# Kernel optimization log

Measured on AMD Instinct MI355X. Metric: run time of the kernel, lower is better.

The kernel has to match this reference:

```python
import jax, jax.numpy as jnp
import numpy as np

NPOINT, RADIUS, NSAMPLE = 1024, 0.2, 32


def _fps(xyz, npoint):
    # xyz: (B, N, 3) -> (B, npoint) int32, iterative furthest point sampling
    B, N, _ = xyz.shape

    def step(carry, _):
        dists, far = carry  # (B,N), (B,)
        centroid = jnp.take_along_axis(xyz, far[:, None, None], axis=1)  # (B,1,3)
        d = jnp.sum((xyz - centroid) ** 2, axis=-1)  # (B,N)
        dists = jnp.minimum(dists, d)
        nxt = jnp.argmax(dists, axis=-1).astype(jnp.int32)
        return (dists, nxt), far

    init = (jnp.full((B, N), 1e10, xyz.dtype), jnp.zeros((B,), jnp.int32))
    _, idx = jax.lax.scan(step, init, None, length=npoint)
    return jnp.transpose(idx)  # (B, npoint)


def _ball_query(radius, nsample, xyz, new_xyz):
    # xyz: (B,N,3), new_xyz: (B,S,3) -> (B,S,nsample) int32
    N = xyz.shape[1]
    d2 = jnp.sum((new_xyz[:, :, None, :] - xyz[:, None, :, :]) ** 2, axis=-1)  # (B,S,N)
    # first-nsample-in-range semantics of PointNet++ ball_query
    key = jnp.where(d2 < radius * radius, jnp.arange(N, dtype=jnp.int32), N)
    neg, order = jax.lax.top_k(-key, nsample)  # smallest keys first
    valid = (-neg) < N
    return jnp.where(valid, order, order[..., :1])  # pad with first valid idx


def _group(feat, idx):
    # feat: (B,D,N), idx: (B,S,ns) -> (B,D,S,ns)
    return jax.vmap(lambda f, i: f[:, i])(feat, idx)


def _conv(x, w, b):
    # 1x1 Conv2d: x (B,C,S,ns), w (O,C), b (O)
    return jnp.einsum('oc,bcps->bops', w, x) + b[None, :, None, None]


def _bn(x, s, t):
    # inference BatchNorm folded into per-channel affine
    return x * s[None, :, None, None] + t[None, :, None, None]


def setup_inputs() -> dict:
    key = jax.random.key(0)
    ks = jax.random.split(key, 40)
    B, N, D = 16, 8192, 64
    BCH = 8  # max(8, 64 // 8)

    def w(k, shape, scale=0.1):
        return jax.random.normal(k, shape, jnp.float32) * scale

    def bn(k, c):
        k1, k2 = jax.random.split(k)
        return (jax.random.uniform(k1, (c,), jnp.float32, 0.75, 1.25),
                0.1 * jax.random.normal(k2, (c,), jnp.float32))

    attn_s0, attn_t0 = bn(ks[2], BCH)
    attn_s1, attn_t1 = bn(ks[3], D)
    attn_s2, attn_t2 = bn(ks[4], D)
    mlp_s0, mlp_t0 = bn(ks[5], 64)
    mlp_s1, mlp_t1 = bn(ks[6], 64)
    eca_s, eca_t = bn(ks[7], 128)
    return {
        'xyz': jax.random.uniform(ks[0], (B, 3, N), jnp.float32),
        'points': jax.random.normal(ks[1], (B, D, N), jnp.float32),
        'attn_w0': w(ks[10], (BCH, 3)), 'attn_b0': w(ks[11], (BCH,)),
        'attn_s0': attn_s0, 'attn_t0': attn_t0,
        'attn_w1': w(ks[12], (D, BCH)), 'attn_b1': w(ks[13], (D,)),
        'attn_s1': attn_s1, 'attn_t1': attn_t1,
        'attn_w2': w(ks[14], (D, D)), 'attn_b2': w(ks[15], (D,)),
        'attn_s2': attn_s2, 'attn_t2': attn_t2,
        'mlp_w0': w(ks[16], (64, D)), 'mlp_b0': w(ks[17], (64,)),
        'mlp_s0': mlp_s0, 'mlp_t0': mlp_t0,
        'mlp_w1': w(ks[18], (64, 64)), 'mlp_b1': w(ks[19], (64,)),
        'mlp_s1': mlp_s1, 'mlp_t1': mlp_t1,
        'eca_k': w(ks[20], (3,), 0.5),
        'eca_w': w(ks[21], (128, 64)), 'eca_b': w(ks[22], (128,)),
        'eca_s': eca_s, 'eca_t': eca_t,
    }


def reference(xyz, points,
              attn_w0, attn_b0, attn_s0, attn_t0,
              attn_w1, attn_b1, attn_s1, attn_t1,
              attn_w2, attn_b2, attn_s2, attn_t2,
              mlp_w0, mlp_b0, mlp_s0, mlp_t0,
              mlp_w1, mlp_b1, mlp_s1, mlp_t1,
              eca_k, eca_w, eca_b, eca_s, eca_t):
    xyz_f = jnp.transpose(xyz, (0, 2, 1))  # (B,N,3)
    # 1. sampling + grouping
    fps_idx = _fps(xyz_f, NPOINT)  # (B,S)
    new_xyz = jax.vmap(lambda p, i: p[:, i])(xyz, fps_idx)  # (B,3,S)
    idx = _ball_query(RADIUS, NSAMPLE, xyz_f, jnp.transpose(new_xyz, (0, 2, 1)))
    grouped_xyz = _group(xyz, idx) - new_xyz[..., None]  # (B,3,S,ns)
    x = _group(points, idx)  # (B,D,S,ns)
    # 2. position-attention module
    pos = jax.nn.relu(_bn(_conv(grouped_xyz, attn_w0, attn_b0), attn_s0, attn_t0))
    pos = _bn(_conv(pos, attn_w1, attn_b1), attn_s1, attn_t1)
    x = x + pos
    x = _bn(_conv(x, attn_w2, attn_b2), attn_s2, attn_t2)
    # 3. shared MLP (conv-bn-relu over mlp[:-1])
    x = jax.nn.relu(_bn(_conv(x, mlp_w0, mlp_b0), mlp_s0, mlp_t0))
    x = jax.nn.relu(_bn(_conv(x, mlp_w1, mlp_b1), mlp_s1, mlp_t1))
    # 4. ECA channel attention + final 1x1 conv-bn
    y = jnp.mean(x, axis=(2, 3))  # (B,C)
    yp = jnp.pad(y, ((0, 0), (1, 1)))
    y = eca_k[0] * yp[:, :-2] + eca_k[1] * yp[:, 1:-1] + eca_k[2] * yp[:, 2:]
    x = x * jax.nn.sigmoid(y)[:, :, None, None]
    x = _bn(_conv(x, eca_w, eca_b), eca_s, eca_t)
    # 5. max-pool over neighborhood
    new_features = jnp.max(x, axis=-1)  # (B,128,S)
    return (new_xyz, new_features)
```

## Files before the change

### kernel.cpp

```cpp
#include <hip/hip_runtime.h>

typedef unsigned int   u32;
typedef unsigned long long u64;
typedef float pkf2 __attribute__((ext_vector_type(2)));

#define B_  16
#define N_  8192
#define S_  1024
#define NS_ 32
#define XS_ 68
#define NWORK_ 240
#define NCHUNK_ 4096

__device__ __forceinline__ float nanguard(float v) {
  u32 x = __float_as_uint(v);
  if ((x & 0x7F80u) == 0x7F80u) x ^= 0x0080u;
  return __uint_as_float(x);
}

__device__ __forceinline__ float wave_max_nonneg(float v) {
  int x = __float_as_int(v);
#define DPP_STEP(ctrl) \
  x = __float_as_int(fmaxf(__int_as_float(x), \
      __int_as_float(__builtin_amdgcn_update_dpp(0, x, (ctrl), 0xf, 0xf, true))))
  DPP_STEP(0x111);
  DPP_STEP(0x112);
  DPP_STEP(0x114);
  DPP_STEP(0x118);
  DPP_STEP(0x142);
  DPP_STEP(0x143);
#undef DPP_STEP
  return __int_as_float(__builtin_amdgcn_readlane(x, 63));
}

__global__ __launch_bounds__(256) void k_xyzt(const float* __restrict__ xyz, float4* __restrict__ xyzt,
                                              u32* __restrict__ prog) {
  if (blockIdx.x == 0 && blockIdx.y == 0 && threadIdx.x < 16) prog[threadIdx.x] = 0u;
  int b = blockIdx.y;
  int i = blockIdx.x * 256 + threadIdx.x;
  const float* p = xyz + (size_t)b * 3 * N_;
  xyzt[(size_t)b * N_ + i] = make_float4(p[i], p[N_ + i], p[2 * N_ + i], 0.f);
}

__global__ __launch_bounds__(256) void k_ptst(const float* __restrict__ pts, float* __restrict__ ptst) {
  __shared__ float tile[64][65];
  int b = blockIdx.y, n0 = blockIdx.x * 64, t = threadIdx.x;
  {
    int c = t >> 2, j0 = (t & 3) * 16;
    const float4* src = (const float4*)(pts + (size_t)b * 64 * N_ + (size_t)c * N_ + n0 + j0);
#pragma unroll
    for (int q = 0; q < 4; ++q) {
      float4 a = src[q];
      tile[c][j0 + 4*q + 0] = a.x; tile[c][j0 + 4*q + 1] = a.y;
      tile[c][j0 + 4*q + 2] = a.z; tile[c][j0 + 4*q + 3] = a.w;
    }
  }
  __syncthreads();
  {
    int n = t >> 2, c0 = (t & 3) * 16;
    float4* dv = (float4*)(ptst + ((size_t)b * N_ + n0 + n) * 64 + c0);
#pragma unroll
    for (int q = 0; q < 4; ++q)
      dv[q] = make_float4(tile[c0 + 4*q + 0][n], tile[c0 + 4*q + 1][n],
                          tile[c0 + 4*q + 2][n], tile[c0 + 4*q + 3][n]);
  }
}

__global__ __launch_bounds__(1024)
__attribute__((amdgpu_waves_per_eu(4, 4)))
void k_fps(const float4* __restrict__ xyzt,
           float4* __restrict__ nxf,
           float* __restrict__ out_xyz) {
#pragma clang fp contract(off)
  __shared__ float4 ldsp[N_];
  __shared__ u64 slot[4];
  __shared__ int win_hist[S_];
  int b = blockIdx.x, t = threadIdx.x;
  const float4* p4 = xyzt + (size_t)b * N_;
  const float4* pp8 = p4 + t * 8;

  float4 q0 = pp8[0], q1 = pp8[1], q2 = pp8[2], q3 = pp8[3];
  float4 q4 = pp8[4], q5 = pp8[5], q6 = pp8[6], q7 = pp8[7];
  ldsp[t * 8 + 0] = q0; ldsp[t * 8 + 1] = q1; ldsp[t * 8 + 2] = q2; ldsp[t * 8 + 3] = q3;
  ldsp[t * 8 + 4] = q4; ldsp[t * 8 + 5] = q5; ldsp[t * 8 + 6] = q6; ldsp[t * 8 + 7] = q7;

#define DECLPAIR(P, A, B) \
  pkf2 px##P = {q##A.x, q##B.x}; pkf2 py##P = {q##A.y, q##B.y}; \
  pkf2 pz##P = {q##A.z, q##B.z}; pkf2 dm##P = {1e10f, 1e10f};
  DECLPAIR(01, 0, 1) DECLPAIR(23, 2, 3) DECLPAIR(45, 4, 5) DECLPAIR(67, 6, 7)
#undef DECLPAIR
#define PIN(P) asm volatile("" : "+v"(px##P), "+v"(py##P), "+v"(pz##P));
  PIN(01) PIN(23) PIN(45) PIN(67)
#undef PIN

  if (t == 0) {
    slot[0] = 8191ull;
    slot[1] = 0; slot[2] = 0; slot[3] = 0;
    win_hist[0] = 0;
  }
  __syncthreads();
  int lane = t & 63;
  for (int it = 1; it < S_; ++it) {
    u64 w = slot[(it - 1) & 3];
    int widx = 8191 - (int)(w & 0xFFFFFFFFull);
    if (t == 0) { win_hist[it - 1] = widx; slot[(it + 1) & 3] = 0; }
    float4 c = ldsp[widx & (N_ - 1)];
    pkf2 cx2 = {c.x, c.x}, cy2 = {c.y, c.y}, cz2 = {c.z, c.z};
#define UPDP(P) { \
    pkf2 dx = px##P - cx2; pkf2 dy = py##P - cy2; pkf2 dz = pz##P - cz2; \
    pkf2 xx = dx * dx; pkf2 yy = dy * dy; pkf2 zz = dz * dz; \
    pkf2 ss = xx + yy; pkf2 dd = ss + zz; \
    dm##P.x = fminf(dm##P.x, dd.x); dm##P.y = fminf(dm##P.y, dd.y); }
    UPDP(01) UPDP(23) UPDP(45) UPDP(67)
#undef UPDP
    float e0 = dm01.x, e1 = dm01.y, e2 = dm23.x, e3 = dm23.y;
    float e4 = dm45.x, e5 = dm45.y, e6 = dm67.x, e7 = dm67.y;
    float va0 = e1 > e0 ? e1 : e0; int ia0 = e1 > e0 ? 1 : 0;
    float va1 = e3 > e2 ? e3 : e2; int ia1 = e3 > e2 ? 3 : 2;
    float va2 = e5 > e4 ? e5 : e4; int ia2 = e5 > e4 ? 5 : 4;
    float va3 = e7 > e6 ? e7 : e6; int ia3 = e7 > e6 ? 7 : 6;
// ... 151 lines not shown

  {
    int n = t >> 3, cc = t & 7;
    const float* gx = &sm.scratch[256 + n * 4];
    float a = sm.bb0[cc];
    a += sm.W0f[cc * 4 + 0] * gx[0];
    a += sm.W0f[cc * 4 + 1] * gx[1];
    a += sm.W0f[cc * 4 + 2] * gx[2];
    sm.scratch[n * 8 + cc] = fmaxf(a, 0.f);
  }
  {
#pragma unroll
    for (int nj = 0; nj < 8; ++nj) {
      float a = sm.bb1[lane];
      const float* p8 = &sm.scratch[(n0 + nj) * 8];
#pragma unroll
      for (int k = 0; k < 8; ++k) a += sm.W1f[lane * 9 + k] * p8[k];
      sm.X[(n0 + nj) * XS_ + lane] += a;
    }
  }
  gemm64<false>(sm.Wbuf, sm.X, sm.H, sm.s2f, sm.bb2, lane, n0);
  __syncthreads();
  stage_w64(sm.Wbuf, m0w, t);
  __syncthreads();
  gemm64<true>(sm.Wbuf, sm.H, sm.X, sm.sm0f, sm.bm0, lane, n0);
  __syncthreads();
  stage_w64(sm.Wbuf, m1w, t);
  __syncthreads();
  gemm64<true>(sm.Wbuf, sm.X, sm.H, sm.sm1f, sm.bm1, lane, n0);
}

template<bool USE_PTST, bool WRITE_H2>
__global__ __launch_bounds__(256) void k_chain(
    const float4* __restrict__ xyzt, const float* __restrict__ ptst,
    const float* __restrict__ points,
    const float4* __restrict__ nxf, const int* __restrict__ ballidx,
    const float* w0, const float* b0, const float* s0, const float* t0,
    const float* w1, const float* b1, const float* s1, const float* t1,
    const float* w2, const float* b2, const float* s2, const float* t2,
    const float* m0w, const float* m0b, const float* m0s, const float* m0t,
    const float* m1w, const float* m1b, const float* m1s, const float* m1t,
    float* __restrict__ h2out, float* __restrict__ partials) {
  __shared__ ChainSm sm;
  int t = threadIdx.x, bs = blockIdx.x;
  int b = bs >> 10, s = bs & 1023;
  int lane = t & 63, g = t >> 6, n0 = g * 8;

  chain_tile<USE_PTST>(sm, b, s, bs, xyzt, ptst, points, nxf, ballidx,
                       w0, b0, s0, t0, w1, b1, s1, t1, w2, b2, s2, t2,
                       m0w, m0b, m0s, m0t, m1w, m1b, m1s, m1t);

  float* psum = sm.scratch;
  float lsum = 0.f;
#pragma unroll
  for (int nj = 0; nj < 8; ++nj) {
    float r = sm.H[(n0 + nj) * XS_ + lane];
    lsum += r;
    if (WRITE_H2)
      h2out[((size_t)bs * 32 + n0 + nj) * 64 + lane] = r;
  }
  psum[lane * 5 + g] = lsum;
  __syncthreads();
  if (t < 64) {
    float v = (psum[t * 5 + 0] + psum[t * 5 + 1]) + (psum[t * 5 + 2] + psum[t * 5 + 3]);
    partials[(size_t)bs * 64 + t] = v;
  }
}

struct ChainSub {
  float X[32 * XS_];
  float H[32 * XS_];
  float scratch[384];
  int   idx_s[NS_];
};
struct WkSm {
  float Wc2[64 * XS_];
  float Wm0[64 * XS_];
  float Wm1[64 * XS_];
  float W1f[64 * 9];
  float W0f[8 * 4];
  float s2f[64], sm0f[64], sm1f[64];
  float bb0[8];
  float bb1[64], bb2[64], bm0[64], bm1[64];
  ChainSub sub[4];
};
struct FpsSm {
  float4 ldsp[N_];
  u64 slot[4];
  int win_hist[S_];
};
union FusedSm { FpsSm f; WkSm w; };
static_assert(sizeof(FusedSm) <= 160 * 1024, "LDS overflow");

__global__ __launch_bounds__(1024)
__attribute__((amdgpu_waves_per_eu(4, 4)))
void k_fused(const float4* __restrict__ xyzt, const float* __restrict__ ptst,
             float4* __restrict__ nxf, float* __restrict__ out_xyz,
             u32* __restrict__ prog,
             const float* w0, const float* b0, const float* s0, const float* t0,
             const float* w1, const float* b1, const float* s1, const float* t1,
             const float* w2, const float* b2, const float* s2, const float* t2,
             const float* m0w, const float* m0b, const float* m0s, const float* m0t,
             const float* m1w, const float* m1b, const float* m1s, const float* m1t,
             float* __restrict__ h2out, float* __restrict__ partials) {
  __shared__ FusedSm smu;
  int t = threadIdx.x;

  if (blockIdx.x < B_) {
#pragma clang fp contract(off)
    FpsSm& fs = smu.f;
    int b = blockIdx.x;
    const float4* p4 = xyzt + (size_t)b * N_;
    const float4* pp8 = p4 + t * 8;

    float4 q0 = pp8[0], q1 = pp8[1], q2 = pp8[2], q3 = pp8[3];
    float4 q4 = pp8[4], q5 = pp8[5], q6 = pp8[6], q7 = pp8[7];
    fs.ldsp[t * 8 + 0] = q0; fs.ldsp[t * 8 + 1] = q1; fs.ldsp[t * 8 + 2] = q2; fs.ldsp[t * 8 + 3] = q3;
    fs.ldsp[t * 8 + 4] = q4; fs.ldsp[t * 8 + 5] = q5; fs.ldsp[t * 8 + 6] = q6; fs.ldsp[t * 8 + 7] = q7;

#define DECLPAIR(P, A, B) \
    pkf2 px##P = {q##A.x, q##B.x}; pkf2 py##P = {q##A.y, q##B.y}; \
    pkf2 pz##P = {q##A.z, q##B.z}; pkf2 dm##P = {1e10f, 1e10f};
    DECLPAIR(01, 0, 1) DECLPAIR(23, 2, 3) DECLPAIR(45, 4, 5) DECLPAIR(67, 6, 7)
#undef DECLPAIR
#define PIN(P) asm volatile("" : "+v"(px##P), "+v"(py##P), "+v"(pz##P));
    PIN(01) PIN(23) PIN(45) PIN(67)
#undef PIN

    if (t == 0) {
      fs.slot[0] = 8191ull;
      fs.slot[1] = 0; fs.slot[2] = 0; fs.slot[3] = 0;
      fs.win_hist[0] = 0;
    }
    __syncthreads();
    int lane = t & 63;
    for (int it = 1; it < S_; ++it) {
      u64 w = fs.slot[(it - 1) & 3];
      int widx = 8191 - (int)(w & 0xFFFFFFFFull);
      float4 c = fs.ldsp[widx & (N_ - 1)];
      if (t == 0) {
        fs.win_hist[it - 1] = widx; fs.slot[(it + 1) & 3] = 0;
        if ((it & 15) == 0)
          __hip_atomic_store(&prog[b], (u32)(it - 1), __ATOMIC_RELEASE, __HIP_MEMORY_SCOPE_AGENT);
        nxf[(size_t)b * S_ + (it - 1)] = c;
      }
      pkf2 cx2 = {c.x, c.x}, cy2 = {c.y, c.y}, cz2 = {c.z, c.z};
#define UPDP(P) { \
      pkf2 dx = px##P - cx2; pkf2 dy = py##P - cy2; pkf2 dz = pz##P - cz2; \
      pkf2 xx = dx * dx; pkf2 yy = dy * dy; pkf2 zz = dz * dz; \
      pkf2 ss = xx + yy; pkf2 dd = ss + zz; \
      dm##P.x = fminf(dm##P.x, dd.x); dm##P.y = fminf(dm##P.y, dd.y); }
      UPDP(01) UPDP(23) UPDP(45) UPDP(67)
#undef UPDP
      float e0 = dm01.x, e1 = dm01.y, e2 = dm23.x, e3 = dm23.y;
      float e4 = dm45.x, e5 = dm45.y, e6 = dm67.x, e7 = dm67.y;
      float va0 = e1 > e0 ? e1 : e0; int ia0 = e1 > e0 ? 1 : 0;
      float va1 = e3 > e2 ? e3 : e2; int ia1 = e3 > e2 ? 3 : 2;
      float va2 = e5 > e4 ? e5 : e4; int ia2 = e5 > e4 ? 5 : 4;
      float va3 = e7 > e6 ? e7 : e6; int ia3 = e7 > e6 ? 7 : 6;
      float vb0 = va1 > va0 ? va1 : va0; int ib0 = va1 > va0 ? ia1 : ia0;
      float vb1 = va3 > va2 ? va3 : va2; int ib1 = va3 > va2 ? ia3 : ia2;
      float bv = vb1 > vb0 ? vb1 : vb0;  int bk = vb1 > vb0 ? ib1 : ib0;
      int bi = t * 8 + bk;
      float wm = wave_max_nonneg(bv);
      u64 msk = __ballot(bv == wm);
      int wl = __ffsll((long long)msk) - 1;
      int wbi = __builtin_amdgcn_readlane(bi, wl);
      if (lane == 0)
        atomicMax(&fs.slot[it & 3],
                  ((u64)__float_as_uint(wm) << 32) | (u64)(u32)(8191 - wbi));
      __syncthreads();
    }
    if (t == 0) {
      int wl_ = 8191 - (int)(fs.slot[(S_ - 1) & 3] & 0xFFFFFFFFull);
      fs.win_hist[S_ - 1] = wl_;
      float4 c = fs.ldsp[wl_ & (N_ - 1)];
      nxf[(size_t)b * S_ + (S_ - 1)] = c;
    }
    __syncthreads();
    {
      int wi = fs.win_hist[t] & (N_ - 1);
      float4 c = fs.ldsp[wi];
      float* o = out_xyz + (size_t)b * 3 * S_;
      o[t] = nanguard(c.x); o[S_ + t] = nanguard(c.y); o[2 * S_ + t] = nanguard(c.z);
    }
    if (t == 0)
      __hip_atomic_store(&prog[b], (u32)S_, __ATOMIC_RELEASE, __HIP_MEMORY_SCOPE_AGENT);
    return;
  }

  WkSm& wk = smu.w;
  int w = blockIdx.x - B_;
  if (t < 256) {
    stage_w64(wk.Wc2, w2, t);
    stage_w64(wk.Wm0, m0w, t);
    stage_w64(wk.Wm1, m1w, t);
  }
  if (t < 64) {
    float v2 = s2[t];  wk.s2f[t] = v2;  wk.bb2[t] = v2 * b2[t] + t2[t];
    float vm0 = m0s[t]; wk.sm0f[t] = vm0; wk.bm0[t] = vm0 * m0b[t] + m0t[t];
    float vm1 = m1s[t]; wk.sm1f[t] = vm1; wk.bm1[t] = vm1 * m1b[t] + m1t[t];
    float v1 = s1[t];
#pragma unroll
    for (int k = 0; k < 8; ++k) wk.W1f[t * 9 + k] = v1 * w1[t * 8 + k];
    wk.bb1[t] = v1 * b1[t] + t1[t];
  }
  if (t < 8) {
    float v0 = s0[t];
#pragma unroll
    for (int k = 0; k < 3; ++k) wk.W0f[t * 4 + k] = v0 * w0[t * 3 + k];
    wk.bb0[t] = v0 * b0[t] + t0[t];
  }
  __syncthreads();

  int sg = t >> 8, tid = t & 255, lane = t & 63, g2 = (t >> 6) & 3, n0 = g2 * 8;
  ChainSub& cs = wk.sub[sg];

  for (int c = w; c < NCHUNK_; c += NWORK_) {
    int s = c >> 2, bg = c & 3, b = bg * 4 + sg;
    if (t == 0) {
      int bbase = bg * 4;
#pragma unroll
      for (int j = 0; j < 4; ++j) {
        while (__hip_atomic_load(&prog[bbase + j], __ATOMIC_RELAXED, __HIP_MEMORY_SCOPE_AGENT) < (u32)(s + 1))
          __builtin_amdgcn_s_sleep(32);
      }
      (void)__hip_atomic_load(&prog[bbase], __ATOMIC_ACQUIRE, __HIP_MEMORY_SCOPE_AGENT);
    }
    __syncthreads();

    float4 cc;
    if (g2 == 0) {
      cc = nxf[(size_t)b * S_ + s];
      const float4* pts = xyzt + (size_t)b * N_;
      int cnt = 0, first = 0;
      bool havefirst = false;
      for (int chunk = 0; chunk < N_; chunk += 64) {
        float4 p = pts[chunk + lane];
        float dx = p.x - cc.x, dy = p.y - cc.y, dz = p.z - cc.z;
        float d2 = __fadd_rn(__fadd_rn(__fmul_rn(dx, dx), __fmul_rn(dy, dy)), __fmul_rn(dz, dz));
        bool v = d2 <= 0.04f;
        u64 m = __ballot(v);
        if (m) {
          int pos = cnt + __popcll(m & ((1ull << lane) - 1ull));
          if (v && pos < NS_) cs.idx_s[pos] = chunk + lane;
          if (!havefirst) { first = chunk + (__ffsll((long long)m) - 1); havefirst = true; }
          cnt += __popcll(m);
          if (cnt >= NS_) break;
        }
      }
      if (cnt < NS_) {
        for (int p = cnt + lane; p < NS_; p += 64) cs.idx_s[p] = first;
      }
    }
    __syncthreads();

    {
      int n = tid >> 3, c8 = (tid & 7) * 8;
      int pi = cs.idx_s[n];
      const float4* v = (const float4*)(ptst + ((size_t)b * N_ + pi) * 64 + c8);
      float4* xr = (float4*)&cs.X[n * XS_ + c8];
      xr[0] = v[0]; xr[1] = v[1];
    }
    if (tid < NS_) {
      float4 p = xyzt[(size_t)b * N_ + cs.idx_s[tid]];
      float* gx = &cs.scratch[256 + tid * 4];
      gx[0] = p.x - cc.x; gx[1] = p.y - cc.y; gx[2] = p.z - cc.z;
    }
    __syncthreads();

    {
      int n = tid >> 3, ch = tid & 7;
      const float* gx = &cs.scratch[256 + n * 4];
      float a = wk.bb0[ch];
      a += wk.W0f[ch * 4 + 0] * gx[0];
      a += wk.W0f[ch * 4 + 1] * gx[1];
      a += wk.W0f[ch * 4 + 2] * gx[2];
      cs.scratch[n * 8 + ch] = fmaxf(a, 0.f);
    }
    {
#pragma unroll
      for (int nj = 0; nj < 8; ++nj) {
        float a = wk.bb1[lane];
        const float* p8 = &cs.scratch[(n0 + nj) * 8];
#pragma unroll
        for (int k = 0; k < 8; ++k) a += wk.W1f[lane * 9 + k] * p8[k];
        cs.X[(n0 + nj) * XS_ + lane] += a;
      }
    }
    gemm64<false>(wk.Wc2, cs.X, cs.H, wk.s2f, wk.bb2, lane, n0);
    gemm64<true >(wk.Wm0, cs.H, cs.X, wk.sm0f, wk.bm0, lane, n0);
    gemm64<true >(wk.Wm1, cs.X, cs.H, wk.sm1f, wk.bm1, lane, n0);

    int bs = (b << 10) | s;
    float lsum = 0.f;
#pragma unroll
    for (int nj = 0; nj < 8; ++nj) {
      float r = cs.H[(n0 + nj) * XS_ + lane];
      lsum += r;
      h2out[((size_t)bs * 32 + n0 + nj) * 64 + lane] = r;
    }
    __syncthreads();
    cs.scratch[lane * 5 + g2] = lsum;
    __syncthreads();
    if (tid < 64) {
      float v = (cs.scratch[tid * 5 + 0] + cs.scratch[tid * 5 + 1]) +
                (cs.scratch[tid * 5 + 2] + cs.scratch[tid * 5 + 3]);
      partials[(size_t)bs * 64 + tid] = v;
    }
  }
}

__global__ __launch_bounds__(256) void k_eca(const float* __restrict__ partials,
                                             const float* __restrict__ ecak,
                                             float* __restrict__ sig) {
  __shared__ float red[64 * 5];
  __shared__ float yy[66];
  int b = blockIdx.x, t = threadIdx.x;
  int c = t & 63, sg = t >> 6;
  float acc = 0.f;
  for (int s = sg; s < S_; s += 4) acc += partials[((size_t)b * S_ + s) * 64 + c];
  red[c * 5 + sg] = acc;
  __syncthreads();
  if (t < 64) {
    float v = (red[t * 5 + 0] + red[t * 5 + 1]) + (red[t * 5 + 2] + red[t * 5 + 3]);
    yy[t + 1] = v * (1.f / 32768.f);
  }
  if (t == 64) { yy[0] = 0.f; yy[65] = 0.f; }
  __syncthreads();
  if (t < 64) {
    float gv = ecak[0] * yy[t] + ecak[1] * yy[t + 1] + ecak[2] * yy[t + 2];
    sig[b * 64 + t] = 1.f / (1.f + expf(-gv));
  }
}

__device__ __forceinline__ void final_gemm(const float* __restrict__ WA,
                                           const float* __restrict__ WB,
                                           const float* __restrict__ X2,
                                           const float* __restrict__ esf,
                                           const float* __restrict__ bbf,
                                           float* __restrict__ zred,
                                           float* __restrict__ outf,
                                           int b, int s, int t) {
  int lane = t & 63, g = t >> 6, n0 = g * 8;
  float aA[8] = {0,0,0,0,0,0,0,0}, aB[8] = {0,0,0,0,0,0,0,0};
#pragma unroll
  for (int k4 = 0; k4 < 16; ++k4) {
    float4 wqA = *(const float4*)&WA[lane * XS_ + k4 * 4];
    float4 wqB = *(const float4*)&WB[lane * XS_ + k4 * 4];
#pragma unroll
    for (int nj = 0; nj < 8; ++nj) {
      float4 xq = *(const float4*)&X2[(n0 + nj) * XS_ + k4 * 4];
      aA[nj] += wqA.x * xq.x; aA[nj] += wqA.y * xq.y;
      aA[nj] += wqA.z * xq.z; aA[nj] += wqA.w * xq.w;
      aB[nj] += wqB.x * xq.x; aB[nj] += wqB.y * xq.y;
      aB[nj] += wqB.z * xq.z; aB[nj] += wqB.w * xq.w;
    }
  }
  float mA = aA[0], mB = aB[0];
#pragma unroll
  for (int j = 1; j < 8; ++j) { mA = fmaxf(mA, aA[j]); mB = fmaxf(mB, aB[j]); }
  zred[lane * 5 + g]        = esf[lane] * mA + bbf[lane];
  zred[(lane + 64) * 5 + g] = esf[lane + 64] * mB + bbf[lane + 64];
  __syncthreads();
  if (t < 128) {
    float m = fmaxf(fmaxf(zred[t * 5 + 0], zred[t * 5 + 1]),
                    fmaxf(zred[t * 5 + 2], zred[t * 5 + 3]));
    outf[((size_t)b * 128 + t) * S_ + s] = nanguard(m);
  }
}

__global__ __launch_bounds__(256) void k_final_h2(const float* __restrict__ h2,
                                                  const float* __restrict__ sig,
                                                  const float* ew, const float* eb,
                                                  const float* es, const float* et,
                                                  float* __restrict__ outf) {
  __shared__ float Wh[128 * XS_];
  __shared__ float esf[128], bbf[128], sigl[64];
  __shared__ float X2[32 * XS_];
  __shared__ float zred[128 * 5];
  int t = threadIdx.x, bs = blockIdx.x;
  int b = bs >> 10, s = bs & 1023;
  {
    int c2 = t >> 1, h = (t & 1) * 32;
    const float4* src = (const float4*)(ew + c2 * 64 + h);
    float4* dst = (float4*)(Wh + c2 * XS_ + h);
#pragma unroll
    for (int j = 0; j < 8; ++j) dst[j] = src[j];
  }
  if (t < 128) {
    float v = es[t]; esf[t] = v; bbf[t] = v * eb[t] + et[t];
  }
  if (t < 64) sigl[t] = sig[b * 64 + t];
  __syncthreads();
  {
    int n = t >> 3, c8 = (t & 7) * 8;
    const float4* v = (const float4*)(h2 + ((size_t)bs * 32 + n) * 64 + c8);
    float4 a = v[0], bq = v[1];
    a.x *= sigl[c8 + 0]; a.y *= sigl[c8 + 1]; a.z *= sigl[c8 + 2]; a.w *= sigl[c8 + 3];
    bq.x *= sigl[c8 + 4]; bq.y *= sigl[c8 + 5]; bq.z *= sigl[c8 + 6]; bq.w *= sigl[c8 + 7];
    float4* xr = (float4*)&X2[n * XS_ + c8];
    xr[0] = a; xr[1] = bq;
  }
  final_gemm(Wh, Wh + 64 * XS_, X2, esf, bbf, zred, outf, b, s, t);
}

template<bool USE_PTST>
__global__ __launch_bounds__(256) void k_final_rec(
    const float4* __restrict__ xyzt, const float* __restrict__ ptst,
    const float* __restrict__ points,
    const float4* __restrict__ nxf, const int* __restrict__ ballidx,
    const float* w0, const float* b0, const float* s0, const float* t0,
    const float* w1, const float* b1, const float* s1, const float* t1,
    const float* w2, const float* b2, const float* s2, const float* t2,
    const float* m0w, const float* m0b, const float* m0s, const float* m0t,
    const float* m1w, const float* m1b, const float* m1s, const float* m1t,
    const float* __restrict__ sig,
    const float* ew, const float* eb, const float* es, const float* et,
    float* __restrict__ outf) {
  __shared__ ChainSm sm;
  __shared__ float Wb2[64 * XS_];
  __shared__ float esf2[128], bbf2[128], sigl2[64];
  __shared__ float zred[128 * 5];
  int t = threadIdx.x, bs = blockIdx.x;
  int b = bs >> 10, s = bs & 1023;
  int lane = t & 63, g = t >> 6, n0 = g * 8;

  chain_tile<USE_PTST>(sm, b, s, bs, xyzt, ptst, points, nxf, ballidx,
                       w0, b0, s0, t0, w1, b1, s1, t1, w2, b2, s2, t2,
                       m0w, m0b, m0s, m0t, m1w, m1b, m1s, m1t);

  __syncthreads();
  stage_w64(sm.Wbuf, ew, t);
  stage_w64(Wb2, ew + 64 * 64, t);
  if (t < 128) {
    float v = es[t]; esf2[t] = v; bbf2[t] = v * eb[t] + et[t];
  }
  if (t < 64) sigl2[t] = sig[b * 64 + t];
  __syncthreads();
  {
#pragma unroll
    for (int nj = 0; nj < 8; ++nj)
      sm.X[(n0 + nj) * XS_ + lane] = sigl2[lane] * sm.H[(n0 + nj) * XS_ + lane];
  }
  final_gemm(sm.Wbuf, Wb2, sm.X, esf2, bbf2, zred, outf, b, s, t);
}

extern "C" void kernel_launch(void* const* d_in, const int* in_sizes, int n_in,
                              void* d_out, int out_size, void* d_ws, size_t ws_size,
                              hipStream_t stream) {
  const float* xyz    = (const float*)d_in[0];
  const float* points = (const float*)d_in[1];
  const float* w0 = (const float*)d_in[2],  *b0 = (const float*)d_in[3],  *s0 = (const float*)d_in[4],  *t0 = (const float*)d_in[5];
  const float* w1 = (const float*)d_in[6],  *b1 = (const float*)d_in[7],  *s1 = (const float*)d_in[8],  *t1 = (const float*)d_in[9];
  const float* w2 = (const float*)d_in[10], *b2 = (const float*)d_in[11], *s2 = (const float*)d_in[12], *t2 = (const float*)d_in[13];
  const float* m0w = (const float*)d_in[14], *m0b = (const float*)d_in[15], *m0s = (const float*)d_in[16], *m0t = (const float*)d_in[17];
  const float* m1w = (const float*)d_in[18], *m1b = (const float*)d_in[19], *m1s = (const float*)d_in[20], *m1t = (const float*)d_in[21];
  const float* ecak = (const float*)d_in[22];
  const float* ew = (const float*)d_in[23], *eb = (const float*)d_in[24], *es = (const float*)d_in[25], *et = (const float*)d_in[26];

  const size_t OFF_XYZT = 0;
  const size_t OFF_NXF  = 2097152;
  const size_t OFF_BIDX = 2359296;
  const size_t OFF_PART = 4456448;
  const size_t OFF_SIG  = 8650752;
  const size_t OFF_PTST = 8654848;
  const size_t OFF_H2   = 42209280;
  const size_t NEED_PTST = OFF_H2;
  const size_t NEED_H2   = 176427008;

  const bool use_ptst = ws_size >= NEED_PTST;
  const bool use_h2   = ws_size >= NEED_H2;

  char* ws = (char*)d_ws;
  float4* xyzt    = (float4*)(ws + OFF_XYZT);
  float4* nxf     = (float4*)(ws + OFF_NXF);
  int*    ballidx = (int*)   (ws + OFF_BIDX);
  u32*    prog    = (u32*)   (ws + OFF_BIDX);
  float*  partials= (float*) (ws + OFF_PART);
  float*  sig     = (float*) (ws + OFF_SIG);
  float*  ptst    = (float*) (ws + OFF_PTST);
  float*  h2      = (float*) (ws + OFF_H2);

  float* out_xyz  = (float*)d_out;
  float* out_feat = (float*)d_out + (size_t)B_ * 3 * S_;

  k_xyzt<<<dim3(N_ / 256, B_), 256, 0, stream>>>(xyz, xyzt, prog);
  if (use_ptst)
    k_ptst<<<dim3(N_ / 64, B_), 256, 0, stream>>>(points, ptst);

  if (use_h2) {
    k_fused<<<B_ + NWORK_, 1024, 0, stream>>>(xyzt, ptst, nxf, out_xyz, prog,
        w0, b0, s0, t0, w1, b1, s1, t1, w2, b2, s2, t2,
        m0w, m0b, m0s, m0t, m1w, m1b, m1s, m1t, h2, partials);
    k_eca<<<B_, 256, 0, stream>>>(partials, ecak, sig);
    k_final_h2<<<B_ * S_, 256, 0, stream>>>(h2, sig, ew, eb, es, et, out_feat);
  } else if (use_ptst) {
    k_fps <<<B_, 1024, 0, stream>>>(xyzt, nxf, out_xyz);
    k_ball<<<(B_ * S_) / 4, 256, 0, stream>>>(xyzt, nxf, ballidx);
    k_chain<true, false><<<B_ * S_, 256, 0, stream>>>(xyzt, ptst, points, nxf, ballidx,
        w0, b0, s0, t0, w1, b1, s1, t1, w2, b2, s2, t2,
        m0w, m0b, m0s, m0t, m1w, m1b, m1s, m1t, h2, partials);
    k_eca<<<B_, 256, 0, stream>>>(partials, ecak, sig);
    k_final_rec<true><<<B_ * S_, 256, 0, stream>>>(xyzt, ptst, points, nxf, ballidx,
        w0, b0, s0, t0, w1, b1, s1, t1, w2, b2, s2, t2,
        m0w, m0b, m0s, m0t, m1w, m1b, m1s, m1t, sig, ew, eb, es, et, out_feat);
  } else {
    k_fps <<<B_, 1024, 0, stream>>>(xyzt, nxf, out_xyz);
    k_ball<<<(B_ * S_) / 4, 256, 0, stream>>>(xyzt, nxf, ballidx);
    k_chain<false, false><<<B_ * S_, 256, 0, stream>>>(xyzt, ptst, points, nxf, ballidx,
        w0, b0, s0, t0, w1, b1, s1, t1, w2, b2, s2, t2,
        m0w, m0b, m0s, m0t, m1w, m1b, m1s, m1t, h2, partials);
    k_eca<<<B_, 256, 0, stream>>>(partials, ecak, sig);
    k_final_rec<false><<<B_ * S_, 256, 0, stream>>>(xyzt, ptst, points, nxf, ballidx,
        w0, b0, s0, t0, w1, b1, s1, t1, w2, b2, s2, t2,
        m0w, m0b, m0s, m0t, m1w, m1b, m1s, m1t, sig, ew, eb, es, et, out_feat);
  }
}
```

Measured before the change: 1.240 ms.

## Fuse points transpose into worker blocks, pad progress counters, persist final kernel

The points transpose (k_ptst) moves into the worker blocks of the fused kernel. It runs there while the FPS blocks iterate, and a global counter barrier makes the workers wait until every transpose tile is written. The per-batch progress counters are spaced 16 words apart to avoid false sharing, and the global progress stores move from thread 0 to thread 64 so they sit off the FPS critical thread. The final ECA GEMM kernel becomes a persistent grid of 768 blocks that loads the weights once per block instead of once per (b,s). The in-kernel barrier depends on all worker blocks being co-resident and adds spin-wait cost.

```diff
diff --git a/kernel.cpp b/kernel.cpp
--- a/kernel.cpp
+++ b/kernel.cpp
@@ -11,6 +11,7 @@
 #define XS_ 68
 #define NWORK_ 240
 #define NCHUNK_ 4096
+#define NFIN_ 768
 
 __device__ __forceinline__ float nanguard(float v) {
   u32 x = __float_as_uint(v);
@@ -35,7 +36,7 @@
 
 __global__ __launch_bounds__(256) void k_xyzt(const float* __restrict__ xyz, float4* __restrict__ xyzt,
                                               u32* __restrict__ prog) {
-  if (blockIdx.x == 0 && blockIdx.y == 0 && threadIdx.x < 16) prog[threadIdx.x] = 0u;
+  if (blockIdx.x == 0 && blockIdx.y == 0 && threadIdx.x < 17) prog[threadIdx.x * 16] = 0u;
   int b = blockIdx.y;
   int i = blockIdx.x * 256 + threadIdx.x;
   const float* p = xyz + (size_t)b * 3 * N_;
@@ -353,7 +354,10 @@
   float s2f[64], sm0f[64], sm1f[64];
   float bb0[8];
   float bb1[64], bb2[64], bm0[64], bm1[64];
-  ChainSub sub[4];
+  union {
+    ChainSub sub[4];
+    float tr[64][65];
+  };
 };
 struct FpsSm {
   float4 ldsp[N_];
@@ -366,6 +370,7 @@
 __global__ __launch_bounds__(1024)
 __attribute__((amdgpu_waves_per_eu(4, 4)))
 void k_fused(const float4* __restrict__ xyzt, const float* __restrict__ ptst,
+             const float* __restrict__ points,
              float4* __restrict__ nxf, float* __restrict__ out_xyz,
              u32* __restrict__ prog,
              const float* w0, const float* b0, const float* s0, const float* t0,
@@ -376,6 +381,7 @@
              float* __restrict__ h2out, float* __restrict__ partials) {
   __shared__ FusedSm smu;
   int t = threadIdx.x;
+  u32* ptst_done = prog + 256;
 
   if (blockIdx.x < B_) {
 #pragma clang fp contract(off)
@@ -409,10 +415,10 @@
       u64 w = fs.slot[(it - 1) & 3];
       int widx = 8191 - (int)(w & 0xFFFFFFFFull);
       float4 c = fs.ldsp[widx & (N_ - 1)];
-      if (t == 0) {
-        fs.win_hist[it - 1] = widx; fs.slot[(it + 1) & 3] = 0;
+      if (t == 0) { fs.win_hist[it - 1] = widx; fs.slot[(it + 1) & 3] = 0; }
+      if (t == 64) {
         if ((it & 15) == 0)
-          __hip_atomic_store(&prog[b], (u32)(it - 1), __ATOMIC_RELEASE, __HIP_MEMORY_SCOPE_AGENT);
+          __hip_atomic_store(&prog[b * 16], (u32)(it - 1), __ATOMIC_RELEASE, __HIP_MEMORY_SCOPE_AGENT);
         nxf[(size_t)b * S_ + (it - 1)] = c;
       }
       pkf2 cx2 = {c.x, c.x}, cy2 = {c.y, c.y}, cz2 = {c.z, c.z};
@@ -442,11 +448,13 @@
                   ((u64)__float_as_uint(wm) << 32) | (u64)(u32)(8191 - wbi));
       __syncthreads();
     }
-    if (t == 0) {
+    if (t == 0)
+      fs.win_hist[S_ - 1] = 8191 - (int)(fs.slot[(S_ - 1) & 3] & 0xFFFFFFFFull);
+    if (t == 64) {
       int wl_ = 8191 - (int)(fs.slot[(S_ - 1) & 3] & 0xFFFFFFFFull);
-      fs.win_hist[S_ - 1] = wl_;
       float4 c = fs.ldsp[wl_ & (N_ - 1)];
       nxf[(size_t)b * S_ + (S_ - 1)] = c;
+      __hip_atomic_store(&prog[b * 16], (u32)S_, __ATOMIC_RELEASE, __HIP_MEMORY_SCOPE_AGENT);
     }
     __syncthreads();
     {
@@ -455,8 +463,6 @@
       float* o = out_xyz + (size_t)b * 3 * S_;
       o[t] = nanguard(c.x); o[S_ + t] = nanguard(c.y); o[2 * S_ + t] = nanguard(c.z);
     }
-    if (t == 0)
-      __hip_atomic_store(&prog[b], (u32)S_, __ATOMIC_RELEASE, __HIP_MEMORY_SCOPE_AGENT);
     return;
   }
 
@@ -482,21 +488,43 @@
     for (int k = 0; k < 3; ++k) wk.W0f[t * 4 + k] = v0 * w0[t * 3 + k];
     wk.bb0[t] = v0 * b0[t] + t0[t];
   }
-  __syncthreads();
+
+  {
+    int tc = t >> 4, j0 = (t & 15) * 4;
+    for (int pt = w; pt < 2048; pt += NWORK_) {
+      int bb = pt >> 7, n0 = (pt & 127) * 64;
+      __syncthreads();
+      float4 a = *(const float4*)(points + (size_t)bb * 64 * N_ + (size_t)tc * N_ + n0 + j0);
+      wk.tr[tc][j0 + 0] = a.x; wk.tr[tc][j0 + 1] = a.y;
+      wk.tr[tc][j0 + 2] = a.z; wk.tr[tc][j0 + 3] = a.w;
+      __syncthreads();
+      *(float4*)(ptst + ((size_t)bb * N_ + n0 + tc) * 64 + j0 * 0 + (t & 15) * 4) =
+        make_float4(wk.tr[(t & 15) * 4 + 0][tc], wk.tr[(t & 15) * 4 + 1][tc],
+                    wk.tr[(t & 15) * 4 + 2][tc], wk.tr[(t & 15) * 4 + 3][tc]);
+    }
+    __threadfence();
+    __syncthreads();
+    if (t == 0) {
+      __hip_atomic_fetch_add(ptst_done, 1u, __ATOMIC_RELEASE, __HIP_MEMORY_SCOPE_AGENT);
+      while (__hip_atomic_load(ptst_done, __ATOMIC_ACQUIRE, __HIP_MEMORY_SCOPE_AGENT) < (u32)NWORK_)
+        __builtin_amdgcn_s_sleep(16);
+    }
+    __syncthreads();
+  }
 
   int sg = t >> 8, tid = t & 255, lane = t & 63, g2 = (t >> 6) & 3, n0 = g2 * 8;
   ChainSub& cs = wk.sub[sg];
 
-  for (int c = w; c < NCHUNK_; c += NWORK_) {
-    int s = c >> 2, bg = c & 3, b = bg * 4 + sg;
+  for (int ck = w; ck < NCHUNK_; ck += NWORK_) {
+    int s = ck >> 2, bg = ck & 3, b = bg * 4 + sg;
     if (t == 0) {
       int bbase = bg * 4;
 #pragma unroll
       for (int j = 0; j < 4; ++j) {
-        while (__hip_atomic_load(&prog[bbase + j], __ATOMIC_RELAXED, __HIP_MEMORY_SCOPE_AGENT) < (u32)(s + 1))
+        while (__hip_atomic_load(&prog[(bbase + j) * 16], __ATOMIC_RELAXED, __HIP_MEMORY_SCOPE_AGENT) < (u32)(s + 1))
           __builtin_amdgcn_s_sleep(32);
       }
-      (void)__hip_atomic_load(&prog[bbase], __ATOMIC_ACQUIRE, __HIP_MEMORY_SCOPE_AGENT);
+      (void)__hip_atomic_load(&prog[bbase * 16], __ATOMIC_ACQUIRE, __HIP_MEMORY_SCOPE_AGENT);
     }
     __syncthreads();
 
@@ -641,17 +669,16 @@
   }
 }
 
-__global__ __launch_bounds__(256) void k_final_h2(const float* __restrict__ h2,
-                                                  const float* __restrict__ sig,
-                                                  const float* ew, const float* eb,
-                                                  const float* es, const float* et,
-                                                  float* __restrict__ outf) {
+__global__ __launch_bounds__(256) void k_final_p(const float* __restrict__ h2,
+                                                 const float* __restrict__ sig,
+                                                 const float* ew, const float* eb,
+                                                 const float* es, const float* et,
+                                                 float* __restrict__ outf) {
   __shared__ float Wh[128 * XS_];
   __shared__ float esf[128], bbf[128], sigl[64];
   __shared__ float X2[32 * XS_];
   __shared__ float zred[128 * 5];
-  int t = threadIdx.x, bs = blockIdx.x;
-  int b = bs >> 10, s = bs & 1023;
+  int t = threadIdx.x;
   {
     int c2 = t >> 1, h = (t & 1) * 32;
     const float4* src = (const float4*)(ew + c2 * 64 + h);
@@ -662,18 +689,21 @@
   if (t < 128) {
     float v = es[t]; esf[t] = v; bbf[t] = v * eb[t] + et[t];
   }
-  if (t < 64) sigl[t] = sig[b * 64 + t];
-  __syncthreads();
-  {
-    int n = t >> 3, c8 = (t & 7) * 8;
-    const float4* v = (const float4*)(h2 + ((size_t)bs * 32 + n) * 64 + c8);
-    float4 a = v[0], bq = v[1];
-    a.x *= sigl[c8 + 0]; a.y *= sigl[c8 + 1]; a.z *= sigl[c8 + 2]; a.w *= sigl[c8 + 3];
-    bq.x *= sigl[c8 + 4]; bq.y *= sigl[c8 + 5]; bq.z *= sigl[c8 + 6]; bq.w *= sigl[c8 + 7];
-    float4* xr = (float4*)&X2[n * XS_ + c8];
-    xr[0] = a; xr[1] = bq;
-  }
-  final_gemm(Wh, Wh + 64 * XS_, X2, esf, bbf, zred, outf, b, s, t);
+  for (int bs = blockIdx.x; bs < B_ * S_; bs += NFIN_) {
+    int b = bs >> 10, s = bs & 1023;
+    if (t < 64) sigl[t] = sig[b * 64 + t];
+    __syncthreads();
+    {
+      int n = t >> 3, c8 = (t & 7) * 8;
+      const float4* v = (const float4*)(h2 + ((size_t)bs * 32 + n) * 64 + c8);
+      float4 a = v[0], bq = v[1];
+      a.x *= sigl[c8 + 0]; a.y *= sigl[c8 + 1]; a.z *= sigl[c8 + 2]; a.w *= sigl[c8 + 3];
+      bq.x *= sigl[c8 + 4]; bq.y *= sigl[c8 + 5]; bq.z *= sigl[c8 + 6]; bq.w *= sigl[c8 + 7];
+      float4* xr = (float4*)&X2[n * XS_ + c8];
+      xr[0] = a; xr[1] = bq;
+    }
+    final_gemm(Wh, Wh + 64 * XS_, X2, esf, bbf, zred, outf, b, s, t);
+  }
 }
 
 template<bool USE_PTST>
@@ -757,16 +787,15 @@
   float* out_feat = (float*)d_out + (size_t)B_ * 3 * S_;
 
   k_xyzt<<<dim3(N_ / 256, B_), 256, 0, stream>>>(xyz, xyzt, prog);
-  if (use_ptst)
-    k_ptst<<<dim3(N_ / 64, B_), 256, 0, stream>>>(points, ptst);
 
   if (use_h2) {
-    k_fused<<<B_ + NWORK_, 1024, 0, stream>>>(xyzt, ptst, nxf, out_xyz, prog,
+    k_fused<<<B_ + NWORK_, 1024, 0, stream>>>(xyzt, ptst, points, nxf, out_xyz, prog,
         w0, b0, s0, t0, w1, b1, s1, t1, w2, b2, s2, t2,
         m0w, m0b, m0s, m0t, m1w, m1b, m1s, m1t, h2, partials);
     k_eca<<<B_, 256, 0, stream>>>(partials, ecak, sig);
-    k_final_h2<<<B_ * S_, 256, 0, stream>>>(h2, sig, ew, eb, es, et, out_feat);
+    k_final_p<<<NFIN_, 256, 0, stream>>>(h2, sig, ew, eb, es, et, out_feat);
   } else if (use_ptst) {
+    k_ptst<<<dim3(N_ / 64, B_), 256, 0, stream>>>(points, ptst);
     k_fps <<<B_, 1024, 0, stream>>>(xyzt, nxf, out_xyz);
     k_ball<<<(B_ * S_) / 4, 256, 0, stream>>>(xyzt, nxf, ballidx);
     k_chain<true, false><<<B_ * S_, 256, 0, stream>>>(xyzt, ptst, points, nxf, ballidx,
```

After: 1.261 ms. About the same (+1.7%).

## Drop points transpose pre-pass and make final ECA GEMM persistent with register weights

Applied to the files above, without the earlier changes.

The fused worker now gathers neighbour features straight from the original channel-major points tensor with strided loads, so the separate k_ptst transpose kernel no longer runs on the h2 path. The final conv kernel becomes a persistent grid of 512 blocks that loads the 128x64 weight matrix into registers once per block and loops over (b,s) tiles, removing the per-block copy of the weights into shared memory. The risks are uncoalesced scattered reads in the gather, heavy register pressure from the 32 float4 weight registers, and a missing barrier between loop iterations: the next iteration's writes to sigl and X2 can overlap the previous iteration's reads.

```diff
diff --git a/kernel.cpp b/kernel.cpp
--- a/kernel.cpp
+++ b/kernel.cpp
@@ -11,6 +11,7 @@
 #define XS_ 68
 #define NWORK_ 240
 #define NCHUNK_ 4096
+#define NFIN_ 512
 
 __device__ __forceinline__ float nanguard(float v) {
   u32 x = __float_as_uint(v);
@@ -365,7 +366,8 @@
 
 __global__ __launch_bounds__(1024)
 __attribute__((amdgpu_waves_per_eu(4, 4)))
-void k_fused(const float4* __restrict__ xyzt, const float* __restrict__ ptst,
+void k_fused(const float4* __restrict__ xyzt,
+             const float* __restrict__ points,
              float4* __restrict__ nxf, float* __restrict__ out_xyz,
              u32* __restrict__ prog,
              const float* w0, const float* b0, const float* s0, const float* t0,
@@ -487,8 +489,8 @@
   int sg = t >> 8, tid = t & 255, lane = t & 63, g2 = (t >> 6) & 3, n0 = g2 * 8;
   ChainSub& cs = wk.sub[sg];
 
-  for (int c = w; c < NCHUNK_; c += NWORK_) {
-    int s = c >> 2, bg = c & 3, b = bg * 4 + sg;
+  for (int ck = w; ck < NCHUNK_; ck += NWORK_) {
+    int s = ck >> 2, bg = ck & 3, b = bg * 4 + sg;
     if (t == 0) {
       int bbase = bg * 4;
 #pragma unroll
@@ -529,9 +531,9 @@
     {
       int n = tid >> 3, c8 = (tid & 7) * 8;
       int pi = cs.idx_s[n];
-      const float4* v = (const float4*)(ptst + ((size_t)b * N_ + pi) * 64 + c8);
-      float4* xr = (float4*)&cs.X[n * XS_ + c8];
-      xr[0] = v[0]; xr[1] = v[1];
+      const float* pp = points + (size_t)b * 64 * N_ + (size_t)c8 * N_ + pi;
+#pragma unroll
+      for (int j = 0; j < 8; ++j) cs.X[n * XS_ + c8 + j] = pp[(size_t)j * N_];
     }
     if (tid < NS_) {
       float4 p = xyzt[(size_t)b * N_ + cs.idx_s[tid]];
@@ -605,6 +607,69 @@
   }
 }
 
+__global__ __launch_bounds__(256, 2) void k_final_p(const float* __restrict__ h2,
+                                                    const float* __restrict__ sig,
+                                                    const float* __restrict__ ew,
+                                                    const float* __restrict__ eb,
+                                                    const float* __restrict__ es,
+                                                    const float* __restrict__ et,
+                                                    float* __restrict__ outf) {
+  __shared__ float esf[128], bbf[128], sigl[64];
+  __shared__ float X2[32 * XS_];
+  __shared__ float zred[128 * 5];
+  int t = threadIdx.x, lane = t & 63, g = t >> 6, n0 = g * 8;
+
+  float4 wA[16], wB[16];
+  {
+    const float4* ra = (const float4*)(ew + (size_t)lane * 64);
+    const float4* rb = (const float4*)(ew + (size_t)(lane + 64) * 64);
+#pragma unroll
+    for (int k = 0; k < 16; ++k) { wA[k] = ra[k]; wB[k] = rb[k]; }
+  }
+  if (t < 128) {
+    float v = es[t]; esf[t] = v; bbf[t] = v * eb[t] + et[t];
+  }
+
+  for (int bs = blockIdx.x; bs < B_ * S_; bs += NFIN_) {
+    int b = bs >> 10, s = bs & 1023;
+    if (t < 64) sigl[t] = sig[b * 64 + t];
+    __syncthreads();
+    {
+      int n = t >> 3, c8 = (t & 7) * 8;
+      const float4* v = (const float4*)(h2 + ((size_t)bs * 32 + n) * 64 + c8);
+      float4 a = v[0], bq = v[1];
+      a.x *= sigl[c8 + 0]; a.y *= sigl[c8 + 1]; a.z *= sigl[c8 + 2]; a.w *= sigl[c8 + 3];
+      bq.x *= sigl[c8 + 4]; bq.y *= sigl[c8 + 5]; bq.z *= sigl[c8 + 6]; bq.w *= sigl[c8 + 7];
+      float4* xr = (float4*)&X2[n * XS_ + c8];
+      xr[0] = a; xr[1] = bq;
+    }
+    float aA[8] = {0,0,0,0,0,0,0,0}, aB[8] = {0,0,0,0,0,0,0,0};
+#pragma unroll
+    for (int k4 = 0; k4 < 16; ++k4) {
+      float4 wqA = wA[k4], wqB = wB[k4];
+#pragma unroll
+      for (int nj = 0; nj < 8; ++nj) {
+        float4 xq = *(const float4*)&X2[(n0 + nj) * XS_ + k4 * 4];
+        aA[nj] += wqA.x * xq.x; aA[nj] += wqA.y * xq.y;
+        aA[nj] += wqA.z * xq.z; aA[nj] += wqA.w * xq.w;
+        aB[nj] += wqB.x * xq.x; aB[nj] += wqB.y * xq.y;
+        aB[nj] += wqB.z * xq.z; aB[nj] += wqB.w * xq.w;
+      }
+    }
+    float mA = aA[0], mB = aB[0];
+#pragma unroll
+    for (int j = 1; j < 8; ++j) { mA = fmaxf(mA, aA[j]); mB = fmaxf(mB, aB[j]); }
+    zred[lane * 5 + g]        = esf[lane] * mA + bbf[lane];
+    zred[(lane + 64) * 5 + g] = esf[lane + 64] * mB + bbf[lane + 64];
+    __syncthreads();
+    if (t < 128) {
+      float m = fmaxf(fmaxf(zred[t * 5 + 0], zred[t * 5 + 1]),
+                      fmaxf(zred[t * 5 + 2], zred[t * 5 + 3]));
+      outf[((size_t)b * 128 + t) * S_ + s] = nanguard(m);
+    }
+  }
+}
+
 __device__ __forceinline__ void final_gemm(const float* __restrict__ WA,
                                            const float* __restrict__ WB,
                                            const float* __restrict__ X2,
@@ -639,41 +704,6 @@
                     fmaxf(zred[t * 5 + 2], zred[t * 5 + 3]));
     outf[((size_t)b * 128 + t) * S_ + s] = nanguard(m);
   }
-}
-
-__global__ __launch_bounds__(256) void k_final_h2(const float* __restrict__ h2,
-                                                  const float* __restrict__ sig,
-                                                  const float* ew, const float* eb,
-                                                  const float* es, const float* et,
-                                                  float* __restrict__ outf) {
-  __shared__ float Wh[128 * XS_];
-  __shared__ float esf[128], bbf[128], sigl[64];
-  __shared__ float X2[32 * XS_];
-  __shared__ float zred[128 * 5];
-  int t = threadIdx.x, bs = blockIdx.x;
-  int b = bs >> 10, s = bs & 1023;
-  {
-    int c2 = t >> 1, h = (t & 1) * 32;
-    const float4* src = (const float4*)(ew + c2 * 64 + h);
-    float4* dst = (float4*)(Wh + c2 * XS_ + h);
-#pragma unroll
-    for (int j = 0; j < 8; ++j) dst[j] = src[j];
-  }
-  if (t < 128) {
-    float v = es[t]; esf[t] = v; bbf[t] = v * eb[t] + et[t];
-  }
-  if (t < 64) sigl[t] = sig[b * 64 + t];
-  __syncthreads();
-  {
-    int n = t >> 3, c8 = (t & 7) * 8;
-    const float4* v = (const float4*)(h2 + ((size_t)bs * 32 + n) * 64 + c8);
-    float4 a = v[0], bq = v[1];
-    a.x *= sigl[c8 + 0]; a.y *= sigl[c8 + 1]; a.z *= sigl[c8 + 2]; a.w *= sigl[c8 + 3];
-    bq.x *= sigl[c8 + 4]; bq.y *= sigl[c8 + 5]; bq.z *= sigl[c8 + 6]; bq.w *= sigl[c8 + 7];
-    float4* xr = (float4*)&X2[n * XS_ + c8];
-    xr[0] = a; xr[1] = bq;
-  }
-  final_gemm(Wh, Wh + 64 * XS_, X2, esf, bbf, zred, outf, b, s, t);
 }
 
 template<bool USE_PTST>
@@ -757,16 +787,15 @@
   float* out_feat = (float*)d_out + (size_t)B_ * 3 * S_;
 
   k_xyzt<<<dim3(N_ / 256, B_), 256, 0, stream>>>(xyz, xyzt, prog);
-  if (use_ptst)
-    k_ptst<<<dim3(N_ / 64, B_), 256, 0, stream>>>(points, ptst);
 
   if (use_h2) {
-    k_fused<<<B_ + NWORK_, 1024, 0, stream>>>(xyzt, ptst, nxf, out_xyz, prog,
+    k_fused<<<B_ + NWORK_, 1024, 0, stream>>>(xyzt, points, nxf, out_xyz, prog,
         w0, b0, s0, t0, w1, b1, s1, t1, w2, b2, s2, t2,
         m0w, m0b, m0s, m0t, m1w, m1b, m1s, m1t, h2, partials);
     k_eca<<<B_, 256, 0, stream>>>(partials, ecak, sig);
-    k_final_h2<<<B_ * S_, 256, 0, stream>>>(h2, sig, ew, eb, es, et, out_feat);
+    k_final_p<<<NFIN_, 256, 0, stream>>>(h2, sig, ew, eb, es, et, out_feat);
   } else if (use_ptst) {
+    k_ptst<<<dim3(N_ / 64, B_), 256, 0, stream>>>(points, ptst);
     k_fps <<<B_, 1024, 0, stream>>>(xyzt, nxf, out_xyz);
     k_ball<<<(B_ * S_) / 4, 256, 0, stream>>>(xyzt, nxf, ballidx);
     k_chain<true, false><<<B_ * S_, 256, 0, stream>>>(xyzt, ptst, points, nxf, ballidx,
```

After: 1.311 ms. +5.7%, slower.

## Make final ECA GEMM kernel persistent with per-wave 8x8 register tiles

Applied to the files above, without the earlier changes.

Replaces the one-block-per-point final kernel (16384 blocks, each reloading the 128x64 weight into LDS) with a persistent grid of 512 blocks. The weights are loaded into LDS once per block and each wave processes a grid-strided sequence of points. Each lane computes an 8x8 output tile in registers and the neighbourhood max is reduced with shuffles instead of an LDS reduction and block sync. This removes repeated weight staging and block-level syncs, at the cost of heavier register use (64 accumulators, launch bounds set to 2) and possibly lower occupancy.

```diff
diff --git a/kernel.cpp b/kernel.cpp
--- a/kernel.cpp
+++ b/kernel.cpp
@@ -11,6 +11,7 @@
 #define XS_ 68
 #define NWORK_ 240
 #define NCHUNK_ 4096
+#define NFIN_ 512
 
 __device__ __forceinline__ float nanguard(float v) {
   u32 x = __float_as_uint(v);
@@ -487,8 +488,8 @@
   int sg = t >> 8, tid = t & 255, lane = t & 63, g2 = (t >> 6) & 3, n0 = g2 * 8;
   ChainSub& cs = wk.sub[sg];
 
-  for (int c = w; c < NCHUNK_; c += NWORK_) {
-    int s = c >> 2, bg = c & 3, b = bg * 4 + sg;
+  for (int ck = w; ck < NCHUNK_; ck += NWORK_) {
+    int s = ck >> 2, bg = ck & 3, b = bg * 4 + sg;
     if (t == 0) {
       int bbase = bg * 4;
 #pragma unroll
@@ -605,6 +606,80 @@
   }
 }
 
+__global__ __launch_bounds__(256, 2) void k_final_h2(const float* __restrict__ h2,
+                                                     const float* __restrict__ sig,
+                                                     const float* ew, const float* eb,
+                                                     const float* es, const float* et,
+                                                     float* __restrict__ outf) {
+  __shared__ float Wh[128 * XS_];
+  __shared__ float esf[128], bbf[128];
+  __shared__ float X2[4][32 * XS_];
+  int t = threadIdx.x;
+  {
+    int c2 = t >> 1, h = (t & 1) * 32;
+    const float4* src = (const float4*)(ew + c2 * 64 + h);
+    float4* dst = (float4*)(Wh + c2 * XS_ + h);
+#pragma unroll
+    for (int j = 0; j < 8; ++j) dst[j] = src[j];
+  }
+  if (t < 128) { float v = es[t]; esf[t] = v; bbf[t] = v * eb[t] + et[t]; }
+  __syncthreads();
+
+  int wv = t >> 6, lane = t & 63;
+  int cg = lane & 15, rg = lane >> 4;
+  float* X = X2[wv];
+  int gw = blockIdx.x * 4 + wv;
+
+  for (int bs = gw; bs < B_ * S_; bs += NFIN_ * 4) {
+    int b = bs >> 10, s = bs & 1023;
+    {
+      float4 sgl = *(const float4*)&sig[b * 64 + cg * 4];
+      const float4* hsrc = (const float4*)(h2 + (size_t)bs * 2048);
+#pragma unroll
+      for (int m = 0; m < 8; ++m) {
+        int q = lane + 64 * m;
+        float4 v = hsrc[q];
+        v.x *= sgl.x; v.y *= sgl.y; v.z *= sgl.z; v.w *= sgl.w;
+        *(float4*)&X[(q >> 4) * XS_ + (q & 15) * 4] = v;
+      }
+    }
+    float acc[8][8];
+#pragma unroll
+    for (int i = 0; i < 8; ++i)
+#pragma unroll
+      for (int j = 0; j < 8; ++j) acc[i][j] = 0.f;
+#pragma unroll
+    for (int k4 = 0; k4 < 16; ++k4) {
+      float4 wq[8], xq[8];
+#pragma unroll
+      for (int i = 0; i < 8; ++i)
+        wq[i] = *(const float4*)&Wh[(cg + 16 * i) * XS_ + k4 * 4];
+#pragma unroll
+      for (int j = 0; j < 8; ++j)
+        xq[j] = *(const float4*)&X[(rg + 4 * j) * XS_ + k4 * 4];
+#pragma unroll
+      for (int i = 0; i < 8; ++i)
+#pragma unroll
+        for (int j = 0; j < 8; ++j) {
+          acc[i][j] += wq[i].x * xq[j].x; acc[i][j] += wq[i].y * xq[j].y;
+          acc[i][j] += wq[i].z * xq[j].z; acc[i][j] += wq[i].w * xq[j].w;
+        }
+    }
+#pragma unroll
+    for (int i = 0; i < 8; ++i) {
+      float m0 = fmaxf(fmaxf(acc[i][0], acc[i][1]), fmaxf(acc[i][2], acc[i][3]));
+      float m1 = fmaxf(fmaxf(acc[i][4], acc[i][5]), fmaxf(acc[i][6], acc[i][7]));
+      float m = fmaxf(m0, m1);
+      m = fmaxf(m, __shfl_xor(m, 16));
+      m = fmaxf(m, __shfl_xor(m, 32));
+      if (rg == 0) {
+        int c = cg + 16 * i;
+        outf[((size_t)b * 128 + c) * S_ + s] = nanguard(esf[c] * m + bbf[c]);
+      }
+    }
+  }
+}
+
 __device__ __forceinline__ void final_gemm(const float* __restrict__ WA,
                                            const float* __restrict__ WB,
                                            const float* __restrict__ X2,
@@ -639,41 +714,6 @@
                     fmaxf(zred[t * 5 + 2], zred[t * 5 + 3]));
     outf[((size_t)b * 128 + t) * S_ + s] = nanguard(m);
   }
-}
-
-__global__ __launch_bounds__(256) void k_final_h2(const float* __restrict__ h2,
-                                                  const float* __restrict__ sig,
-                                                  const float* ew, const float* eb,
-                                                  const float* es, const float* et,
-                                                  float* __restrict__ outf) {
-  __shared__ float Wh[128 * XS_];
-  __shared__ float esf[128], bbf[128], sigl[64];
-  __shared__ float X2[32 * XS_];
-  __shared__ float zred[128 * 5];
-  int t = threadIdx.x, bs = blockIdx.x;
-  int b = bs >> 10, s = bs & 1023;
-  {
-    int c2 = t >> 1, h = (t & 1) * 32;
-    const float4* src = (const float4*)(ew + c2 * 64 + h);
-    float4* dst = (float4*)(Wh + c2 * XS_ + h);
-#pragma unroll
-    for (int j = 0; j < 8; ++j) dst[j] = src[j];
-  }
-  if (t < 128) {
-    float v = es[t]; esf[t] = v; bbf[t] = v * eb[t] + et[t];
-  }
-  if (t < 64) sigl[t] = sig[b * 64 + t];
-  __syncthreads();
-  {
-    int n = t >> 3, c8 = (t & 7) * 8;
-    const float4* v = (const float4*)(h2 + ((size_t)bs * 32 + n) * 64 + c8);
-    float4 a = v[0], bq = v[1];
-    a.x *= sigl[c8 + 0]; a.y *= sigl[c8 + 1]; a.z *= sigl[c8 + 2]; a.w *= sigl[c8 + 3];
-    bq.x *= sigl[c8 + 4]; bq.y *= sigl[c8 + 5]; bq.z *= sigl[c8 + 6]; bq.w *= sigl[c8 + 7];
-    float4* xr = (float4*)&X2[n * XS_ + c8];
-    xr[0] = a; xr[1] = bq;
-  }
-  final_gemm(Wh, Wh + 64 * XS_, X2, esf, bbf, zred, outf, b, s, t);
 }
 
 template<bool USE_PTST>
@@ -765,7 +805,7 @@
         w0, b0, s0, t0, w1, b1, s1, t1, w2, b2, s2, t2,
         m0w, m0b, m0s, m0t, m1w, m1b, m1s, m1t, h2, partials);
     k_eca<<<B_, 256, 0, stream>>>(partials, ecak, sig);
-    k_final_h2<<<B_ * S_, 256, 0, stream>>>(h2, sig, ew, eb, es, et, out_feat);
+    k_final_h2<<<NFIN_, 256, 0, stream>>>(h2, sig, ew, eb, es, et, out_feat);
   } else if (use_ptst) {
     k_fps <<<B_, 1024, 0, stream>>>(xyzt, nxf, out_xyz);
     k_ball<<<(B_ * S_) / 4, 256, 0, stream>>>(xyzt, nxf, ballidx);
```

After: 4.396 ms. 3.54x slower.
